# Kernel tuning notes

Measured on AMD Instinct MI355X. Metric: run time of the kernel, lower is better.

Reference implementation:

```python
import jax, jax.numpy as jnp
import numpy as np

SCALE_FLOOR = 0.001
N_SOURCES = 16


def setup_inputs() -> dict:
    key = jax.random.key(0)
    ks = jax.random.split(key, 8)
    n, d_in, d = 131072, 1024, 512
    x = jax.random.normal(ks[0], (n, d_in), dtype=jnp.float32)
    source_ids = jax.random.randint(ks[1], (n,), 0, N_SOURCES, dtype=jnp.int64)
    # backbone: single Linear(d_in -> d)
    Wb = jax.random.normal(ks[2], (d_in, d), dtype=jnp.float32) / np.sqrt(d_in)
    bb = jax.random.normal(ks[3], (d,), dtype=jnp.float32) * 0.01
    # pooled head: Linear(d -> 2)
    Wp = jax.random.normal(ks[4], (d, 2), dtype=jnp.float32) / np.sqrt(d)
    bp = jax.random.normal(ks[5], (2,), dtype=jnp.float32) * 0.01
    # per-source heads stacked: [S, d, 2], [S, 2]
    Ws = jax.random.normal(ks[6], (N_SOURCES, d, 2), dtype=jnp.float32) / np.sqrt(d)
    bs = jax.random.normal(ks[7], (N_SOURCES, 2), dtype=jnp.float32) * 0.01
    return {"x": x, "source_ids": source_ids, "Wb": Wb, "bb": bb,
            "Wp": Wp, "bp": bp, "Ws": Ws, "bs": bs}


def _head(raw):
    # raw: (n, 2) -> (mu, scale) with softplus + floor on scale
    mu = raw[:, 0]
    scale = jax.nn.softplus(raw[:, 1]) + SCALE_FLOOR
    return mu, scale


def reference(x, source_ids, Wb, bb, Wp, bp, Ws, bs):
    # backbone embedding: (n, d)
    emb = x @ Wb + bb
    # pooled head
    pooled_mu, pooled_scale = _head(emb @ Wp + bp)
    # routed per-source heads: compute all tiny heads, then gather per row.
    # raw_all: (n, S, 2); S*2 is tiny so this beats gather of per-row weights.
    raw_all = jnp.einsum('nd,sdk->nsk', emb, Ws) + bs[None, :, :]
    raw_sel = jnp.take_along_axis(raw_all, source_ids[:, None, None], axis=1)[:, 0, :]
    src_mu, src_scale = _head(raw_sel)
    # all source ids fall in [0, N_SOURCES), so every row is covered
    # (matches the torch loop where unmatched rows would stay zero).
    return emb, pooled_mu, pooled_scale, src_mu, src_scale
```

## Files before the change

### kernel.cpp

```cpp
#include <hip/hip_runtime.h>

typedef short bf16x8 __attribute__((ext_vector_type(8)));
typedef float f32x4 __attribute__((ext_vector_type(4)));
typedef unsigned uint4v __attribute__((ext_vector_type(4)));

#define NROWS 131072L
#define DIN 1024
#define DEMB 512
#define NEXT 640

__device__ __forceinline__ unsigned short f2bf(float f) {
  unsigned u = __float_as_uint(f);
  u += 0x7FFFu + ((u >> 16) & 1u);
  return (unsigned short)(u >> 16);
}

__device__ __forceinline__ unsigned pkhi(float a, float b) {
  unsigned ua = __float_as_uint(a) + 0x8000u;
  unsigned ub = __float_as_uint(b) + 0x8000u;
  return __builtin_amdgcn_perm(ub, ua, 0x07060302u);
}

__device__ __forceinline__ float softplusf(float v) {
  return fmaxf(v, 0.f) + log1pf(expf(-fabsf(v)));
}

__global__ __launch_bounds__(256) void wb_transpose(const float* __restrict__ Wb,
                                                    unsigned short* __restrict__ WbT) {
  int g = blockIdx.x * 256 + threadIdx.x;
  int n = g & 511;
  int kb = g >> 9;
  unsigned short tmp[8];
#pragma unroll
  for (int j = 0; j < 8; ++j)
    tmp[j] = f2bf(Wb[(kb * 8 + j) * DEMB + n]);
  uint4 v;
  v.x = (unsigned)tmp[0] | ((unsigned)tmp[1] << 16);
  v.y = (unsigned)tmp[2] | ((unsigned)tmp[3] << 16);
  v.z = (unsigned)tmp[4] | ((unsigned)tmp[5] << 16);
  v.w = (unsigned)tmp[6] | ((unsigned)tmp[7] << 16);
  *(uint4*)(WbT + (long)n * DIN + kb * 8) = v;
}

__global__ void zero_tail(unsigned* __restrict__ p) {
  p[blockIdx.x * 256 + threadIdx.x] = 0u;
}

__global__ __launch_bounds__(256) void wfold_rows(const float* __restrict__ Wb,
                                                  const float* __restrict__ Wp,
                                                  const float* __restrict__ Ws,
                                                  unsigned short* __restrict__ WbT) {
  int w = threadIdx.x >> 6, lane = threadIdx.x & 63;
  int k = blockIdx.x * 4 + w;
  if (lane >= 34) return;
  const float* src;
  if (lane < 2) src = Wp + lane;
  else { int s = (lane - 2) >> 1; src = Ws + s * 1024 + (lane & 1); }
  const float* wrow = Wb + (long)k * DEMB;
  float acc = 0.f;
#pragma unroll 8
  for (int d = 0; d < DEMB; ++d) acc = fmaf(wrow[d], src[2 * d], acc);
  WbT[(long)(512 + lane) * DIN + k] = f2bf(acc);
}

__global__ void bfold_k(const float* __restrict__ bb, const float* __restrict__ Wp,
                        const float* __restrict__ bp, const float* __restrict__ Ws,
                        const float* __restrict__ bs, float* __restrict__ bf) {
  int j = threadIdx.x;
  if (j >= 34) return;
  const float* src; float bias;
  if (j < 2) { src = Wp + j; bias = bp[j]; }
  else { int s = (j - 2) >> 1; src = Ws + s * 1024 + (j & 1); bias = bs[s * 2 + (j & 1)]; }
  float acc = bias;
  for (int d = 0; d < DEMB; ++d) acc = fmaf(bb[d], src[2 * d], acc);
  bf[j] = acc;
}

__global__ __launch_bounds__(256, 2) void gemm_fused(
    const float* __restrict__ x, const unsigned short* __restrict__ wbt,
    const float* __restrict__ bb, const int* __restrict__ sid,
    const float* __restrict__ bfold, float* __restrict__ out) {
  __shared__ __align__(16) char SM[65536];
  char* const A0 = SM;
  char* const A1 = SM + 16384;
  char* const A2 = SM + 32768;
  char* const B0 = SM + 49152;
  char* const B1 = SM + 57344;

  const int t = threadIdx.x;
  const int lane = t & 63;
  const int wid = t >> 6;
  const int wm = wid >> 1, wn = wid & 1;

  const int bid = blockIdx.x;
  const int swz = (bid & 7) * 640 + (bid >> 3);
  const int mtile = swz / 5;
  const int ntile = swz - mtile * 5;
  const long m0 = (long)mtile * 128;
  const int n0 = ntile * 128;

  const int gswA = (t & 7) ^ ((t >> 3) & 7);
  const float* xA = x + (m0 + (t >> 3)) * DIN + gswA * 4;

  const int bn = wid * 16 + (lane >> 2);
  const int bsg = (lane & 3) ^ ((lane >> 3) & 3);
  const unsigned short* bsrc = wbt + (long)(n0 + bn) * DIN + bsg * 8;

  const int l15 = lane & 15, lg = lane >> 4;
  const int kgoB = ((lg ^ ((l15 >> 1) & 3)) << 4);
  const int brdrow = (wn * 64 + l15) * 64;
  const int arow = (wm * 64 + l15) * 128;
  const int g0x = (((lg * 2) ^ (l15 & 7)) << 4);
  const int g1x = (((lg * 2 + 1) ^ (l15 & 7)) << 4);

  f32x4 acc[4][4] = {};

  auto stageA = [&](char* Aw, int k0) {
#pragma unroll
    for (int p = 0; p < 4; ++p) {
      const float* gp = xA + (long)p * 32 * DIN + k0;
      __builtin_amdgcn_global_load_lds(
          (const __attribute__((address_space(1))) void*)gp,
          (__attribute__((address_space(3))) void*)(Aw + p * 4096 + wid * 1024),
          16, 0, 0);
    }
  };
  auto stageB = [&](char* Bw, int k0) {
#pragma unroll
    for (int i = 0; i < 2; ++i) {
      const unsigned short* gp = bsrc + (long)i * 64 * DIN + k0;
      __builtin_amdgcn_global_load_lds(
          (const __attribute__((address_space(1))) void*)gp,
          (__attribute__((address_space(3))) void*)(Bw + i * 4096 + wid * 1024),
          16, 0, 0);
    }
  };
  auto compute = [&](const char* Ac, const char* Bc) {
    bf16x8 af[4], bfv[4];
#pragma unroll
    for (int i = 0; i < 4; ++i) {
      f32x4 q0 = *(const f32x4*)(Ac + arow + i * 2048 + g0x);
      f32x4 q1 = *(const f32x4*)(Ac + arow + i * 2048 + g1x);
      uint4v u;
      u[0] = pkhi(q0[0], q0[1]); u[1] = pkhi(q0[2], q0[3]);
      u[2] = pkhi(q1[0], q1[1]); u[3] = pkhi(q1[2], q1[3]);
      af[i] = __builtin_bit_cast(bf16x8, u);
      bfv[i] = *(const bf16x8*)(Bc + brdrow + i * 1024 + kgoB);
    }
#pragma unroll
    for (int mi = 0; mi < 4; ++mi)
#pragma unroll
      for (int ni = 0; ni < 4; ++ni)
        acc[mi][ni] = __builtin_amdgcn_mfma_f32_16x16x32_bf16(af[mi], bfv[ni],
                                                             acc[mi][ni], 0, 0, 0);
  };
  auto body = [&](char* Ac, char* Aw, char* Bc, char* Bw, int tt) {
    stageB(Bw, (tt + 1) * 32);
    stageA(Aw, (tt + 2) * 32);
    compute(Ac, Bc);
    __builtin_amdgcn_sched_barrier(0);
    asm volatile("s_waitcnt vmcnt(4) lgkmcnt(0)" ::: "memory");
    __builtin_amdgcn_sched_barrier(0);
    __builtin_amdgcn_s_barrier();
  };

  stageA(A0, 0);
  stageB(B0, 0);
  stageA(A1, 32);
  __builtin_amdgcn_sched_barrier(0);
  asm volatile("s_waitcnt vmcnt(4) lgkmcnt(0)" ::: "memory");
  __builtin_amdgcn_sched_barrier(0);
  __builtin_amdgcn_s_barrier();

#pragma unroll 1
  for (int tb = 0; tb < 30; tb += 6) {
    body(A0, A2, B0, B1, tb + 0);
    body(A1, A0, B1, B0, tb + 1);
    body(A2, A1, B0, B1, tb + 2);
    body(A0, A2, B1, B0, tb + 3);
    body(A1, A0, B0, B1, tb + 4);
    body(A2, A1, B1, B0, tb + 5);
  }
  stageB(B1, 31 * 32);
  compute(A0, B0);
  __builtin_amdgcn_sched_barrier(0);
  asm volatile("s_waitcnt vmcnt(0) lgkmcnt(0)" ::: "memory");
  __builtin_amdgcn_sched_barrier(0);
  __builtin_amdgcn_s_barrier();
  compute(A1, B1);

  if (ntile < 4) {
    const int colg = n0 + wn * 64 + l15;
    float bbv[4];
#pragma unroll
    for (int ni = 0; ni < 4; ++ni) bbv[ni] = bb[colg + ni * 16];
#pragma unroll
    for (int mi = 0; mi < 4; ++mi) {
      const long rbase = m0 + wm * 64 + mi * 16 + lg * 4;
#pragma unroll
      for (int ni = 0; ni < 4; ++ni)
#pragma unroll
        for (int r = 0; r < 4; ++r)
          out[(rbase + r) * DEMB + colg + ni * 16] = acc[mi][ni][r] + bbv[ni];
    }
  } else {
    __syncthreads();
    float* hl = (float*)SM;
    if (wn == 0) {
#pragma unroll
      for (int ni = 0; ni < 3; ++ni)
#pragma unroll
        for (int mi = 0; mi < 4; ++mi)
#pragma unroll
          for (int r = 0; r < 4; ++r) {
            int row = wm * 64 + mi * 16 + lg * 4 + r;
            hl[row * 49 + l15 + ni * 16] = acc[mi][ni][r];
          }
    }
    __syncthreads();
    if (t < 128) {
      const long row = m0 + t;
      const int s = sid[row];
      const float v0 = hl[t * 49 + 0] + bfold[0];
      const float v1 = hl[t * 49 + 1] + bfold[1];
      const float v2 = hl[t * 49 + 2 + 2 * s] + bfold[2 + 2 * s];
      const float v3 = hl[t * 49 + 3 + 2 * s] + bfold[3 + 2 * s];
      float* hp = out + NROWS * DEMB;
      hp[row] = v0;
      hp[NROWS + row] = softplusf(v1) + 0.001f;
      hp[2 * NROWS + row] = v2;
      hp[3 * NROWS + row] = softplusf(v3) + 0.001f;
    }
  }
}

extern "C" void kernel_launch(void* const* d_in, const int* in_sizes, int n_in,
                              void* d_out, int out_size, void* d_ws, size_t ws_size,
                              hipStream_t stream) {
  const float* x  = (const float*)d_in[0];
  const int* sid  = (const int*)d_in[1];
  const float* Wb = (const float*)d_in[2];
  const float* bb = (const float*)d_in[3];
  const float* Wp = (const float*)d_in[4];
  const float* bp = (const float*)d_in[5];
  const float* Ws = (const float*)d_in[6];
  const float* bs = (const float*)d_in[7];
  float* out = (float*)d_out;
  unsigned short* WbT = (unsigned short*)d_ws;
  float* bfoldp = (float*)(WbT + (long)NEXT * DIN);

  wb_transpose<<<256, 256, 0, stream>>>(Wb, WbT);
  zero_tail<<<188, 256, 0, stream>>>((unsigned*)(WbT + 546 * DIN));
  wfold_rows<<<256, 256, 0, stream>>>(Wb, Wp, Ws, WbT);
  bfold_k<<<1, 64, 0, stream>>>(bb, Wp, bp, Ws, bs, bfoldp);
  gemm_fused<<<5120, 256, 0, stream>>>(x, WbT, bb, sid, bfoldp, out);
}
```

Baseline: 366.2 us.

## Load fp32 A tiles directly into registers, shrink LDS to raise occupancy

The fp32 x tiles are no longer staged through LDS with a triple buffer. Each wave now loads its A fragments straight from global memory into registers, double-buffered across iterations. This cuts LDS from 64KB to 18KB and raises the launch bound to 3 blocks per SM, aiming to hide latency through more occupancy and fewer LDS round-trips. The costs are extra register pressure and uncoalesced-ish global reads of x (16 rows × 32 bytes per wave) in place of the swizzled async copy. The head scratch row stride shrinks to 35 floats so it fits the smaller LDS.

```diff
diff --git a/kernel.cpp b/kernel.cpp
--- a/kernel.cpp
+++ b/kernel.cpp
@@ -76,16 +76,13 @@
   bf[j] = acc;
 }
 
-__global__ __launch_bounds__(256, 2) void gemm_fused(
+__global__ __launch_bounds__(256, 3) void gemm_fused(
     const float* __restrict__ x, const unsigned short* __restrict__ wbt,
     const float* __restrict__ bb, const int* __restrict__ sid,
     const float* __restrict__ bfold, float* __restrict__ out) {
-  __shared__ __align__(16) char SM[65536];
-  char* const A0 = SM;
-  char* const A1 = SM + 16384;
-  char* const A2 = SM + 32768;
-  char* const B0 = SM + 49152;
-  char* const B1 = SM + 57344;
+  __shared__ __align__(16) char SM[18432];
+  char* const B0 = SM;
+  char* const B1 = SM + 8192;
 
   const int t = threadIdx.x;
   const int lane = t & 63;
@@ -99,32 +96,20 @@
   const long m0 = (long)mtile * 128;
   const int n0 = ntile * 128;
 
-  const int gswA = (t & 7) ^ ((t >> 3) & 7);
-  const float* xA = x + (m0 + (t >> 3)) * DIN + gswA * 4;
+  const int l15 = lane & 15, lg = lane >> 4;
+
+  const float* xw = x + (m0 + wm * 64 + l15) * DIN + lg * 8;
 
   const int bn = wid * 16 + (lane >> 2);
   const int bsg = (lane & 3) ^ ((lane >> 3) & 3);
   const unsigned short* bsrc = wbt + (long)(n0 + bn) * DIN + bsg * 8;
 
-  const int l15 = lane & 15, lg = lane >> 4;
   const int kgoB = ((lg ^ ((l15 >> 1) & 3)) << 4);
   const int brdrow = (wn * 64 + l15) * 64;
-  const int arow = (wm * 64 + l15) * 128;
-  const int g0x = (((lg * 2) ^ (l15 & 7)) << 4);
-  const int g1x = (((lg * 2 + 1) ^ (l15 & 7)) << 4);
 
   f32x4 acc[4][4] = {};
-
-  auto stageA = [&](char* Aw, int k0) {
-#pragma unroll
-    for (int p = 0; p < 4; ++p) {
-      const float* gp = xA + (long)p * 32 * DIN + k0;
-      __builtin_amdgcn_global_load_lds(
-          (const __attribute__((address_space(1))) void*)gp,
-          (__attribute__((address_space(3))) void*)(Aw + p * 4096 + wid * 1024),
-          16, 0, 0);
-    }
-  };
+  f32x4 arC[4][2], arN[4][2];
+
   auto stageB = [&](char* Bw, int k0) {
 #pragma unroll
     for (int i = 0; i < 2; ++i) {
@@ -135,15 +120,23 @@
           16, 0, 0);
     }
   };
-  auto compute = [&](const char* Ac, const char* Bc) {
+  auto loadA = [&](f32x4 (*d)[2], int k0) {
+#pragma unroll
+    for (int mi = 0; mi < 4; ++mi) {
+      const float* p = xw + (long)mi * 16 * DIN + k0;
+      d[mi][0] = *(const f32x4*)p;
+      d[mi][1] = *(const f32x4*)(p + 4);
+    }
+  };
+  auto compute = [&](const char* Bc, f32x4 (*a)[2]) {
     bf16x8 af[4], bfv[4];
 #pragma unroll
     for (int i = 0; i < 4; ++i) {
-      f32x4 q0 = *(const f32x4*)(Ac + arow + i * 2048 + g0x);
-      f32x4 q1 = *(const f32x4*)(Ac + arow + i * 2048 + g1x);
       uint4v u;
-      u[0] = pkhi(q0[0], q0[1]); u[1] = pkhi(q0[2], q0[3]);
-      u[2] = pkhi(q1[0], q1[1]); u[3] = pkhi(q1[2], q1[3]);
+      u[0] = pkhi(a[i][0][0], a[i][0][1]);
+      u[1] = pkhi(a[i][0][2], a[i][0][3]);
+      u[2] = pkhi(a[i][1][0], a[i][1][1]);
+      u[3] = pkhi(a[i][1][2], a[i][1][3]);
       af[i] = __builtin_bit_cast(bf16x8, u);
       bfv[i] = *(const bf16x8*)(Bc + brdrow + i * 1024 + kgoB);
     }
@@ -154,40 +147,30 @@
         acc[mi][ni] = __builtin_amdgcn_mfma_f32_16x16x32_bf16(af[mi], bfv[ni],
                                                              acc[mi][ni], 0, 0, 0);
   };
-  auto body = [&](char* Ac, char* Aw, char* Bc, char* Bw, int tt) {
+  auto body = [&](char* Bc, char* Bw, f32x4 (*ac)[2], f32x4 (*an)[2], int tt) {
     stageB(Bw, (tt + 1) * 32);
-    stageA(Aw, (tt + 2) * 32);
-    compute(Ac, Bc);
+    loadA(an, (tt + 1) * 32);
+    compute(Bc, ac);
     __builtin_amdgcn_sched_barrier(0);
-    asm volatile("s_waitcnt vmcnt(4) lgkmcnt(0)" ::: "memory");
+    asm volatile("s_waitcnt vmcnt(8) lgkmcnt(0)" ::: "memory");
     __builtin_amdgcn_sched_barrier(0);
     __builtin_amdgcn_s_barrier();
   };
 
-  stageA(A0, 0);
   stageB(B0, 0);
-  stageA(A1, 32);
+  loadA(arC, 0);
   __builtin_amdgcn_sched_barrier(0);
-  asm volatile("s_waitcnt vmcnt(4) lgkmcnt(0)" ::: "memory");
+  asm volatile("s_waitcnt vmcnt(8) lgkmcnt(0)" ::: "memory");
   __builtin_amdgcn_sched_barrier(0);
   __builtin_amdgcn_s_barrier();
 
 #pragma unroll 1
-  for (int tb = 0; tb < 30; tb += 6) {
-    body(A0, A2, B0, B1, tb + 0);
-    body(A1, A0, B1, B0, tb + 1);
-    body(A2, A1, B0, B1, tb + 2);
-    body(A0, A2, B1, B0, tb + 3);
-    body(A1, A0, B0, B1, tb + 4);
-    body(A2, A1, B1, B0, tb + 5);
+  for (int tb = 0; tb < 30; tb += 2) {
+    body(B0, B1, arC, arN, tb);
+    body(B1, B0, arN, arC, tb + 1);
   }
-  stageB(B1, 31 * 32);
-  compute(A0, B0);
-  __builtin_amdgcn_sched_barrier(0);
-  asm volatile("s_waitcnt vmcnt(0) lgkmcnt(0)" ::: "memory");
-  __builtin_amdgcn_sched_barrier(0);
-  __builtin_amdgcn_s_barrier();
-  compute(A1, B1);
+  body(B0, B1, arC, arN, 30);
+  compute(B1, arN);
 
   if (ntile < 4) {
     const int colg = n0 + wn * 64 + l15;
@@ -208,23 +191,26 @@
     float* hl = (float*)SM;
     if (wn == 0) {
 #pragma unroll
-      for (int ni = 0; ni < 3; ++ni)
+      for (int ni = 0; ni < 3; ++ni) {
+        if (ni * 16 + 0 >= 35) continue;
 #pragma unroll
         for (int mi = 0; mi < 4; ++mi)
 #pragma unroll
           for (int r = 0; r < 4; ++r) {
             int row = wm * 64 + mi * 16 + lg * 4 + r;
-            hl[row * 49 + l15 + ni * 16] = acc[mi][ni][r];
+            int col = l15 + ni * 16;
+            if (col < 35) hl[row * 35 + col] = acc[mi][ni][r];
           }
+      }
     }
     __syncthreads();
     if (t < 128) {
       const long row = m0 + t;
       const int s = sid[row];
-      const float v0 = hl[t * 49 + 0] + bfold[0];
-      const float v1 = hl[t * 49 + 1] + bfold[1];
-      const float v2 = hl[t * 49 + 2 + 2 * s] + bfold[2 + 2 * s];
-      const float v3 = hl[t * 49 + 3 + 2 * s] + bfold[3 + 2 * s];
+      const float v0 = hl[t * 35 + 0] + bfold[0];
+      const float v1 = hl[t * 35 + 1] + bfold[1];
+      const float v2 = hl[t * 35 + 2 + 2 * s] + bfold[2 + 2 * s];
+      const float v3 = hl[t * 35 + 3 + 2 * s] + bfold[3 + 2 * s];
       float* hp = out + NROWS * DEMB;
       hp[row] = v0;
       hp[NROWS + row] = softplusf(v1) + 0.001f;
```

Result: slower. 711.7 us (+94.3%).
